# Kernel optimization log

Hardware: AMD Instinct MI355X
Metric: run time of the kernel (lower is better)

## Reference

```python
import jax, jax.numpy as jnp
import numpy as np

NCLASSES = 4
FG_THRESH = 0.5
MEANS = jnp.array([0.0, 0.0, 0.0, 0.0], dtype=jnp.float32)
STDS = jnp.array([0.1, 0.1, 0.2, 0.2], dtype=jnp.float32)
BBOX_INSIDE_W = jnp.array([1.0, 1.0, 1.0, 1.0], dtype=jnp.float32)


def _bbox_overlaps(boxes, gt):
    # boxes: (B,M,4), gt: (B,K,4) -> IoU (B,M,K), faithful to bbox_overlaps_batch
    aw = boxes[..., 2] - boxes[..., 0] + 1.0
    ah = boxes[..., 3] - boxes[..., 1] + 1.0
    gw = gt[..., 2] - gt[..., 0] + 1.0
    gh = gt[..., 3] - gt[..., 1] + 1.0
    area_a = aw * ah                      # (B,M)
    area_g = gw * gh                      # (B,K)
    ix1 = jnp.maximum(boxes[:, :, None, 0], gt[:, None, :, 0])
    iy1 = jnp.maximum(boxes[:, :, None, 1], gt[:, None, :, 1])
    ix2 = jnp.minimum(boxes[:, :, None, 2], gt[:, None, :, 2])
    iy2 = jnp.minimum(boxes[:, :, None, 3], gt[:, None, :, 3])
    iw = jnp.clip(ix2 - ix1 + 1.0, 0.0)
    ih = jnp.clip(iy2 - iy1 + 1.0, 0.0)
    inter = iw * ih                       # (B,M,K)
    ov = inter / (area_a[:, :, None] + area_g[:, None, :] - inter)
    gt_zero = (gw == 1.0) & (gh == 1.0)   # zero-area (padding) gt boxes
    an_zero = (aw == 1.0) & (ah == 1.0)
    ov = jnp.where(gt_zero[:, None, :], 0.0, ov)
    ov = jnp.where(an_zero[:, :, None], -1.0, ov)
    return ov


def _bbox_transform(ex, gt):
    ew = ex[..., 2] - ex[..., 0] + 1.0
    eh = ex[..., 3] - ex[..., 1] + 1.0
    ecx = ex[..., 0] + 0.5 * ew
    ecy = ex[..., 1] + 0.5 * eh
    gw = gt[..., 2] - gt[..., 0] + 1.0
    gh = gt[..., 3] - gt[..., 1] + 1.0
    gcx = gt[..., 0] + 0.5 * gw
    gcy = gt[..., 1] + 0.5 * gh
    dx = (gcx - ecx) / ew
    dy = (gcy - ecy) / eh
    dw = jnp.log(gw / ew)
    dh = jnp.log(gh / eh)
    return jnp.stack([dx, dy, dw, dh], axis=-1)


def setup_inputs() -> dict:
    key = jax.random.key(0)
    B, N, K = 16, 8192, 128
    ks = jax.random.split(key, 9)
    # valid proposal boxes inside an ~1242x375 (KITTI-like) image
    x1 = jax.random.uniform(ks[0], (B, N)) * 1000.0
    y1 = jax.random.uniform(ks[1], (B, N)) * 300.0
    bw = jax.random.uniform(ks[2], (B, N)) * 200.0 + 4.0
    bh = jax.random.uniform(ks[3], (B, N)) * 150.0 + 4.0
    all_rois = jnp.concatenate(
        [jnp.zeros((B, N, 1), jnp.float32),
         jnp.stack([x1, y1, x1 + bw, y1 + bh], axis=-1)], axis=-1)
    gx1 = jax.random.uniform(ks[4], (B, K)) * 1000.0
    gy1 = jax.random.uniform(ks[5], (B, K)) * 300.0
    gw = jax.random.uniform(ks[6], (B, K)) * 200.0 + 8.0
    gh = jax.random.uniform(ks[7], (B, K)) * 150.0 + 8.0
    cls = jax.random.randint(ks[8], (B, K), 1, NCLASSES).astype(jnp.float32)
    gt_boxes = jnp.stack([gx1, gy1, gx1 + gw, gy1 + gh, cls], axis=-1)
    return {"all_rois": all_rois, "gt_boxes": gt_boxes}


def reference(all_rois, gt_boxes):
    B = all_rois.shape[0]
    dt = all_rois.dtype
    # append gt boxes as extra rois: (0, x1, y1, x2, y2)
    gt_append = jnp.concatenate(
        [jnp.zeros_like(gt_boxes[..., :1]), gt_boxes[..., :4]], axis=-1)
    rois = jnp.concatenate([all_rois, gt_append], axis=1)   # (B,M,5)
    M = rois.shape[1]

    ov = _bbox_overlaps(rois[..., 1:5], gt_boxes[..., :4])  # (B,M,K)
    max_ov = ov.max(axis=2)                                 # (B,M)
    gt_assign = jnp.argmax(ov, axis=2)                      # (B,M)
    labels_all = jnp.take_along_axis(gt_boxes[..., 4], gt_assign, axis=1)

    # focal-loss path: fg = ov >= thresh, keep order = [fg asc, bg asc]
    fg = max_ov >= FG_THRESH
    order = jnp.argsort(jnp.where(fg, 0, 1).astype(jnp.int32), axis=1, stable=True)
    fg_count = fg.sum(axis=1)                               # (B,)
    pos = jnp.arange(M)[None, :]

    labels_perm = jnp.take_along_axis(labels_all, order, axis=1)
    labels_batch = jnp.where(pos < fg_count[:, None], labels_perm, 0.0)

    rois_perm = jnp.take_along_axis(rois, order[..., None], axis=1)
    rois_batch = rois_perm.at[..., 0].set(
        jnp.broadcast_to(jnp.arange(B, dtype=dt)[:, None], (B, M)))

    ga_perm = jnp.take_along_axis(gt_assign, order, axis=1)
    gt_rois = jnp.take_along_axis(gt_boxes, ga_perm[..., None], axis=1)  # (B,M,5)

    targets = _bbox_transform(rois_batch[..., 1:5], gt_rois[..., :4])
    targets = (targets - MEANS) / STDS
    bbox_targets = jnp.where((labels_batch > 0)[..., None], targets, 0.0)

    # focal inside weights in ORIGINAL roi order (as in the source), bg zeroed
    focal_w = jnp.where(fg, (1.0 - max_ov) ** 2, 0.0)       # (B,M)
    bbox_inside_weights = jnp.broadcast_to(focal_w[..., None], (B, M, 4))
    bbox_outside_weights = (bbox_inside_weights > 0).astype(dt)

    return (rois_batch, labels_batch, bbox_targets,
            bbox_inside_weights, bbox_outside_weights)
```

## Files before the change

kernel.cpp:

```cpp
#include <hip/hip_runtime.h>
#include <math.h>

#define BB 16
#define NN 8192
#define KK 128
#define MM (NN + KK)
#define NCHUNK 32
#define SENTINEL ((int)0xAAAAAAAA)

__global__ __launch_bounds__(256) void ptl_fused(
    const float* __restrict__ all_rois,
    const float* __restrict__ gt_boxes,
    int* __restrict__ chunk_counts,
    float* __restrict__ out_rois,
    float* __restrict__ out_labels,
    float* __restrict__ out_targets,
    float* __restrict__ out_inside,
    float* __restrict__ out_outside)
{
    __shared__ float4 s_box[KK];
    __shared__ float  s_lbl[KK];
    __shared__ int    s_w[4];
    __shared__ int    s_cnt[NCHUNK];
    __shared__ int    s_gtfg[2];

    const int b    = blockIdx.y;
    const int cx   = blockIdx.x;
    const int tid  = threadIdx.x;
    const int lane = tid & 63, wv = tid >> 6;

    bool nondeg = false;
    if (tid < KK) {
        const float* g = gt_boxes + ((size_t)b * KK + tid) * 5;
        float gx1 = g[0], gy1 = g[1], gx2 = g[2], gy2 = g[3];
        float gw = gx2 - gx1 + 1.0f, gh = gy2 - gy1 + 1.0f;
        bool z = (gw == 1.0f) && (gh == 1.0f);
        nondeg = !z;
        s_box[tid] = z ? make_float4(1e30f, 1e30f, -1e30f, -1e30f)
                       : make_float4(gx1, gy1, gx2 + 1.0f, gy2 + 1.0f);
        s_lbl[tid] = g[4];
    }
    {
        unsigned long long nm = __ballot(nondeg);
        if (wv < 2 && lane == 0) s_gtfg[wv] = __popcll(nm);
    }
    __syncthreads();
    const int gtFg = s_gtfg[0] + s_gtfg[1];

    const int i = cx * 256 + tid;
    const float* rp_in = all_rois + ((size_t)b * NN + i) * 5;
    const float x1 = rp_in[1], y1 = rp_in[2], x2 = rp_in[3], y2 = rp_in[4];
    const float X2p = x2 + 1.0f, Y2p = y2 + 1.0f;
    const float aw = X2p - x1, ah = Y2p - y1;
    const float area_a = aw * ah;

    float best = -1e30f;
    int besti = 0;
    #pragma unroll 4
    for (int k = 0; k < KK; ++k) {
        float4 g = s_box[k];
        float area_g = (g.z - g.x) * (g.w - g.y);
        float iw = fmaxf(fminf(X2p, g.z) - fmaxf(x1, g.x), 0.0f);
        float ih = fmaxf(fminf(Y2p, g.w) - fmaxf(y1, g.y), 0.0f);
        float inter = iw * ih;
        float ov = inter / (area_a + area_g - inter);
        if (ov > best) { best = ov; besti = k; }
    }
    if (aw == 1.0f && ah == 1.0f) { best = -1.0f; besti = 0; }

    const bool fg = (best >= 0.5f);

    unsigned long long m = __ballot(fg ? 1 : 0);
    const int lp = __popcll(m & ((1ull << lane) - 1ull));
    if (lane == 0) s_w[wv] = __popcll(m);
    __syncthreads();
    if (tid == 0) {
        int s = s_w[0] + s_w[1] + s_w[2] + s_w[3];
        __hip_atomic_store(&chunk_counts[b * NCHUNK + cx], s,
                           __ATOMIC_RELAXED, __HIP_MEMORY_SCOPE_AGENT);
    }
    int we = 0;
    for (int w2 = 0; w2 < wv; ++w2) we += s_w[w2];
    const int inChunkExcl = we + lp;

    {
        const size_t idx = (size_t)b * MM + i;
        const float om = 1.0f - best;
        const float w  = fg ? om * om : 0.0f;
        const float ow = (w > 0.0f) ? 1.0f : 0.0f;
        ((float4*)out_inside)[idx]  = make_float4(w, w, w, w);
        ((float4*)out_outside)[idx] = make_float4(ow, ow, ow, ow);
    }
    if (cx == 0 && tid < KK) {
        const size_t idx = (size_t)b * MM + NN + tid;
        ((float4*)out_inside)[idx]  = make_float4(0.f, 0.f, 0.f, 0.f);
        ((float4*)out_outside)[idx] = make_float4(0.f, 0.f, 0.f, 0.f);
    }

    if (tid < 64) {
        const bool need = (lane < NCHUNK);
        int v = SENTINEL;
        if (need)
            v = __hip_atomic_load(&chunk_counts[b * NCHUNK + lane],
                                  __ATOMIC_RELAXED, __HIP_MEMORY_SCOPE_AGENT);
        while (__ballot(need && v == SENTINEL) != 0ull) {
            __builtin_amdgcn_s_sleep(1);
            if (need && v == SENTINEL)
                v = __hip_atomic_load(&chunk_counts[b * NCHUNK + lane],
                                      __ATOMIC_RELAXED, __HIP_MEMORY_SCOPE_AGENT);
        }
        if (need) s_cnt[lane] = v;
    }
    __syncthreads();

    int base = 0, pTotal = 0;
    for (int c = 0; c < NCHUNK; ++c) {
        int v = s_cnt[c];
        pTotal += v;
        if (c < cx) base += v;
    }
    const int total = pTotal + gtFg;

    {
        const int fgBefore = base + inChunkExcl;
        const int p = fg ? fgBefore : (total + i - fgBefore);

        float* rp = out_rois + ((size_t)b * MM + p) * 5;
        rp[0] = (float)b;
        rp[1] = x1; rp[2] = y1; rp[3] = x2; rp[4] = y2;

        float lbl = 0.f;
        float4 t = make_float4(0.f, 0.f, 0.f, 0.f);
        if (fg) {
            lbl = s_lbl[besti];
            if (lbl > 0.0f) {
                float4 g = s_box[besti];
                const float gw = g.z - g.x, gh = g.w - g.y;
                const float gcx = g.x + 0.5f * gw, gcy = g.y + 0.5f * gh;
                const float ew = x2 - x1 + 1.0f, eh = y2 - y1 + 1.0f;
                const float ecx = x1 + 0.5f * ew, ecy = y1 + 0.5f * eh;
                t.x = ((gcx - ecx) / ew) / 0.1f;
                t.y = ((gcy - ecy) / eh) / 0.1f;
                t.z = logf(gw / ew) / 0.2f;
                t.w = logf(gh / eh) / 0.2f;
            }
        }
        out_labels[(size_t)b * MM + p] = lbl;
        ((float4*)out_targets)[(size_t)b * MM + p] = t;
    }

    if (cx == NCHUNK - 1 && tid < KK) {
        const int j = tid;
        const float* g = gt_boxes + ((size_t)b * KK + j) * 5;
        const float gx1 = g[0], gy1 = g[1], gx2 = g[2], gy2 = g[3], cls = g[4];
        const float gw = gx2 - gx1 + 1.0f, gh = gy2 - gy1 + 1.0f;
        const bool nd = !((gw == 1.0f) && (gh == 1.0f));

        unsigned long long m2 = __ballot(nd);
        int pre = __popcll(m2 & ((1ull << lane) - 1ull));
        if (wv == 1) pre += s_gtfg[0];

        const int fgBefore = pTotal + pre;
        const int p = nd ? fgBefore : (total + (NN + j) - fgBefore);

        float* rp = out_rois + ((size_t)b * MM + p) * 5;
        rp[0] = (float)b;
        rp[1] = gx1; rp[2] = gy1; rp[3] = gx2; rp[4] = gy2;
        out_labels[(size_t)b * MM + p] = nd ? cls : 0.0f;
        ((float4*)out_targets)[(size_t)b * MM + p] = make_float4(0.f, 0.f, 0.f, 0.f);
    }
}

extern "C" void kernel_launch(void* const* d_in, const int* in_sizes, int n_in,
                              void* d_out, int out_size, void* d_ws, size_t ws_size,
                              hipStream_t stream) {
    const float* all_rois = (const float*)d_in[0];
    const float* gt_boxes = (const float*)d_in[1];

    float* out = (float*)d_out;
    float* out_rois    = out;
    float* out_labels  = out_rois    + (size_t)BB * MM * 5;
    float* out_targets = out_labels  + (size_t)BB * MM;
    float* out_inside  = out_targets + (size_t)BB * MM * 4;
    float* out_outside = out_inside  + (size_t)BB * MM * 4;

    int* chunk_counts = (int*)d_ws;

    ptl_fused<<<dim3(NCHUNK, BB), dim3(256, 1, 1), 0, stream>>>(
        all_rois, gt_boxes, chunk_counts,
        out_rois, out_labels, out_targets, out_inside, out_outside);
}
```

Measured before the change: 75.46 us.

## Split fused kernel into IoU and scatter kernels, replacing spin-wait sync

```diff
diff --git a/kernel.cpp b/kernel.cpp
--- a/kernel.cpp
+++ b/kernel.cpp
@@ -6,46 +6,33 @@
 #define KK 128
 #define MM (NN + KK)
 #define NCHUNK 32
-#define SENTINEL ((int)0xAAAAAAAA)
-
-__global__ __launch_bounds__(256) void ptl_fused(
+
+
+__global__ __launch_bounds__(256) void ptl_iou(
     const float* __restrict__ all_rois,
     const float* __restrict__ gt_boxes,
     int* __restrict__ chunk_counts,
-    float* __restrict__ out_rois,
-    float* __restrict__ out_labels,
-    float* __restrict__ out_targets,
+    float2* __restrict__ pack,
     float* __restrict__ out_inside,
     float* __restrict__ out_outside)
 {
     __shared__ float4 s_box[KK];
-    __shared__ float  s_lbl[KK];
     __shared__ int    s_w[4];
-    __shared__ int    s_cnt[NCHUNK];
-    __shared__ int    s_gtfg[2];
 
     const int b    = blockIdx.y;
     const int cx   = blockIdx.x;
     const int tid  = threadIdx.x;
     const int lane = tid & 63, wv = tid >> 6;
 
-    bool nondeg = false;
     if (tid < KK) {
         const float* g = gt_boxes + ((size_t)b * KK + tid) * 5;
         float gx1 = g[0], gy1 = g[1], gx2 = g[2], gy2 = g[3];
         float gw = gx2 - gx1 + 1.0f, gh = gy2 - gy1 + 1.0f;
         bool z = (gw == 1.0f) && (gh == 1.0f);
-        nondeg = !z;
         s_box[tid] = z ? make_float4(1e30f, 1e30f, -1e30f, -1e30f)
                        : make_float4(gx1, gy1, gx2 + 1.0f, gy2 + 1.0f);
-        s_lbl[tid] = g[4];
-    }
-    {
-        unsigned long long nm = __ballot(nondeg);
-        if (wv < 2 && lane == 0) s_gtfg[wv] = __popcll(nm);
     }
     __syncthreads();
-    const int gtFg = s_gtfg[0] + s_gtfg[1];
 
     const int i = cx * 256 + tid;
     const float* rp_in = all_rois + ((size_t)b * NN + i) * 5;
@@ -70,19 +57,6 @@
 
     const bool fg = (best >= 0.5f);
 
-    unsigned long long m = __ballot(fg ? 1 : 0);
-    const int lp = __popcll(m & ((1ull << lane) - 1ull));
-    if (lane == 0) s_w[wv] = __popcll(m);
-    __syncthreads();
-    if (tid == 0) {
-        int s = s_w[0] + s_w[1] + s_w[2] + s_w[3];
-        __hip_atomic_store(&chunk_counts[b * NCHUNK + cx], s,
-                           __ATOMIC_RELAXED, __HIP_MEMORY_SCOPE_AGENT);
-    }
-    int we = 0;
-    for (int w2 = 0; w2 < wv; ++w2) we += s_w[w2];
-    const int inChunkExcl = we + lp;
-
     {
         const size_t idx = (size_t)b * MM + i;
         const float om = 1.0f - best;
@@ -97,22 +71,66 @@
         ((float4*)out_outside)[idx] = make_float4(0.f, 0.f, 0.f, 0.f);
     }
 
-    if (tid < 64) {
-        const bool need = (lane < NCHUNK);
-        int v = SENTINEL;
-        if (need)
-            v = __hip_atomic_load(&chunk_counts[b * NCHUNK + lane],
-                                  __ATOMIC_RELAXED, __HIP_MEMORY_SCOPE_AGENT);
-        while (__ballot(need && v == SENTINEL) != 0ull) {
-            __builtin_amdgcn_s_sleep(1);
-            if (need && v == SENTINEL)
-                v = __hip_atomic_load(&chunk_counts[b * NCHUNK + lane],
-                                      __ATOMIC_RELAXED, __HIP_MEMORY_SCOPE_AGENT);
-        }
-        if (need) s_cnt[lane] = v;
-    }
+    pack[(size_t)b * NN + i] = make_float2(best, __int_as_float(besti));
+
+    unsigned long long m = __ballot(fg ? 1 : 0);
+    if (lane == 0) s_w[wv] = __popcll(m);
     __syncthreads();
-
+    if (tid == 0)
+        chunk_counts[b * NCHUNK + cx] = s_w[0] + s_w[1] + s_w[2] + s_w[3];
+}
+
+__global__ __launch_bounds__(256) void ptl_scatter(
+    const float* __restrict__ all_rois,
+    const float* __restrict__ gt_boxes,
+    const int* __restrict__ chunk_counts,
+    const float2* __restrict__ pack,
+    float* __restrict__ out_rois,
+    float* __restrict__ out_labels,
+    float* __restrict__ out_targets)
+{
+    __shared__ float4 s_box[KK];
+    __shared__ float  s_lbl[KK];
+    __shared__ int    s_cnt[NCHUNK];
+    __shared__ int    s_gtfg[2];
+    __shared__ int    s_w[4];
+
+    const int b    = blockIdx.y;
+    const int cx   = blockIdx.x;
+    const int tid  = threadIdx.x;
+    const int lane = tid & 63, wv = tid >> 6;
+
+    bool nondeg = false;
+    if (tid < KK) {
+        const float* g = gt_boxes + ((size_t)b * KK + tid) * 5;
+        float gx1 = g[0], gy1 = g[1], gx2 = g[2], gy2 = g[3];
+        float gw = gx2 - gx1 + 1.0f, gh = gy2 - gy1 + 1.0f;
+        bool z = (gw == 1.0f) && (gh == 1.0f);
+        nondeg = !z;
+        s_box[tid] = z ? make_float4(1e30f, 1e30f, -1e30f, -1e30f)
+                       : make_float4(gx1, gy1, gx2 + 1.0f, gy2 + 1.0f);
+        s_lbl[tid] = g[4];
+    }
+    {
+        unsigned long long nm = __ballot(nondeg);
+        if (wv < 2 && lane == 0) s_gtfg[wv] = __popcll(nm);
+    }
+    if (tid < NCHUNK) s_cnt[tid] = chunk_counts[b * NCHUNK + tid];
+
+    const int i = cx * 256 + tid;
+    const float* rp_in = all_rois + ((size_t)b * NN + i) * 5;
+    const float x1 = rp_in[1], y1 = rp_in[2], x2 = rp_in[3], y2 = rp_in[4];
+    const float2 pk = pack[(size_t)b * NN + i];
+    const float best = pk.x;
+    const int   besti = __float_as_int(pk.y);
+    const bool  fg = (best >= 0.5f);
+
+    unsigned long long m = __ballot(fg ? 1 : 0);
+    const int lp = __popcll(m & ((1ull << lane) - 1ull));
+    if (lane == 0) s_w[wv] = __popcll(m);
+    __syncthreads();
+
+    const int gtFg = s_gtfg[0] + s_gtfg[1];
     int base = 0, pTotal = 0;
     for (int c = 0; c < NCHUNK; ++c) {
         int v = s_cnt[c];
@@ -120,6 +138,10 @@
         if (c < cx) base += v;
     }
     const int total = pTotal + gtFg;
+
+    int we = 0;
+    for (int w2 = 0; w2 < wv; ++w2) we += s_w[w2];
+    const int inChunkExcl = we + lp;
 
     {
         const int fgBefore = base + inChunkExcl;
@@ -184,9 +206,13 @@
     float* out_inside  = out_targets + (size_t)BB * MM * 4;
     float* out_outside = out_inside  + (size_t)BB * MM * 4;
 
-    int* chunk_counts = (int*)d_ws;
-
-    ptl_fused<<<dim3(NCHUNK, BB), dim3(256, 1, 1), 0, stream>>>(
-        all_rois, gt_boxes, chunk_counts,
-        out_rois, out_labels, out_targets, out_inside, out_outside);
+    int*    chunk_counts = (int*)d_ws;
+    float2* pack         = (float2*)((char*)d_ws + 8192);
+
+    ptl_iou<<<dim3(NCHUNK, BB), dim3(256, 1, 1), 0, stream>>>(
+        all_rois, gt_boxes, chunk_counts, pack, out_inside, out_outside);
+
+    ptl_scatter<<<dim3(NCHUNK, BB), dim3(256, 1, 1), 0, stream>>>(
+        all_rois, gt_boxes, chunk_counts, pack,
+        out_rois, out_labels, out_targets);
 }
```

Result: slower. 77.47 us (+2.7%).

## Split IoU gt loop across thread pairs and double chunk count

Applied to the files above, without the earlier changes.

```diff
diff --git a/kernel.cpp b/kernel.cpp
--- a/kernel.cpp
+++ b/kernel.cpp
@@ -5,10 +5,11 @@
 #define NN 8192
 #define KK 128
 #define MM (NN + KK)
-#define NCHUNK 32
+#define NCHUNK 64
+#define RPB 128
 #define SENTINEL ((int)0xAAAAAAAA)
 
-__global__ __launch_bounds__(256) void ptl_fused(
+__global__ __launch_bounds__(256, 6) void ptl_fused(
     const float* __restrict__ all_rois,
     const float* __restrict__ gt_boxes,
     int* __restrict__ chunk_counts,
@@ -28,6 +29,8 @@
     const int cx   = blockIdx.x;
     const int tid  = threadIdx.x;
     const int lane = tid & 63, wv = tid >> 6;
+    const int sub  = tid & 1;
+    const int r    = tid >> 1;
 
     bool nondeg = false;
     if (tid < KK) {
@@ -47,7 +50,7 @@
     __syncthreads();
     const int gtFg = s_gtfg[0] + s_gtfg[1];
 
-    const int i = cx * 256 + tid;
+    const int i = cx * RPB + r;
     const float* rp_in = all_rois + ((size_t)b * NN + i) * 5;
     const float x1 = rp_in[1], y1 = rp_in[2], x2 = rp_in[3], y2 = rp_in[4];
     const float X2p = x2 + 1.0f, Y2p = y2 + 1.0f;
@@ -56,8 +59,10 @@
 
     float best = -1e30f;
     int besti = 0;
+    const int k0 = sub << 6;
     #pragma unroll 4
-    for (int k = 0; k < KK; ++k) {
+    for (int kk = 0; kk < 64; ++kk) {
+        const int k = k0 + kk;
         float4 g = s_box[k];
         float area_g = (g.z - g.x) * (g.w - g.y);
         float iw = fmaxf(fminf(X2p, g.z) - fmaxf(x1, g.x), 0.0f);
@@ -66,11 +71,16 @@
         float ov = inter / (area_a + area_g - inter);
         if (ov > best) { best = ov; besti = k; }
     }
+    {
+        float ob = __shfl_xor(best, 1);
+        int   oi = __shfl_xor(besti, 1);
+        if (ob > best || (ob == best && oi < besti)) { best = ob; besti = oi; }
+    }
     if (aw == 1.0f && ah == 1.0f) { best = -1.0f; besti = 0; }
 
     const bool fg = (best >= 0.5f);
 
-    unsigned long long m = __ballot(fg ? 1 : 0);
+    unsigned long long m = __ballot((fg && sub == 0) ? 1 : 0);
     const int lp = __popcll(m & ((1ull << lane) - 1ull));
     if (lane == 0) s_w[wv] = __popcll(m);
     __syncthreads();
@@ -83,7 +93,7 @@
     for (int w2 = 0; w2 < wv; ++w2) we += s_w[w2];
     const int inChunkExcl = we + lp;
 
-    {
+    if (sub == 0) {
         const size_t idx = (size_t)b * MM + i;
         const float om = 1.0f - best;
         const float w  = fg ? om * om : 0.0f;
@@ -98,18 +108,15 @@
     }
 
     if (tid < 64) {
-        const bool need = (lane < NCHUNK);
-        int v = SENTINEL;
-        if (need)
-            v = __hip_atomic_load(&chunk_counts[b * NCHUNK + lane],
+        int v = __hip_atomic_load(&chunk_counts[b * NCHUNK + lane],
                                   __ATOMIC_RELAXED, __HIP_MEMORY_SCOPE_AGENT);
-        while (__ballot(need && v == SENTINEL) != 0ull) {
+        while (__ballot(v == SENTINEL) != 0ull) {
             __builtin_amdgcn_s_sleep(1);
-            if (need && v == SENTINEL)
+            if (v == SENTINEL)
                 v = __hip_atomic_load(&chunk_counts[b * NCHUNK + lane],
                                       __ATOMIC_RELAXED, __HIP_MEMORY_SCOPE_AGENT);
         }
-        if (need) s_cnt[lane] = v;
+        s_cnt[lane] = v;
     }
     __syncthreads();
 
@@ -121,7 +128,7 @@
     }
     const int total = pTotal + gtFg;
 
-    {
+    if (sub == 0) {
         const int fgBefore = base + inChunkExcl;
         const int p = fg ? fgBefore : (total + i - fgBefore);
 
```

New measurement: 78.30 us. 3.8% more time.
